# Optimization experiments

Hardware: AMD Instinct MI355X
Metric: run time of the kernel (lower is better)

The kernel has to match this reference:

```python
import jax, jax.numpy as jnp
import numpy as np
import math

N_HEADS = 16

def _rope_tables(T, D, dtype):
    # inv_freq over even dims, emb = [freqs, freqs] -> [T, D]
    inv_freq = 1.0 / (10000.0 ** (jnp.arange(0, D, 2, dtype=jnp.float32) / D))
    freqs = jnp.arange(T, dtype=jnp.float32)[:, None] * inv_freq[None, :]  # [T, D/2]
    emb = jnp.concatenate([freqs, freqs], axis=-1)  # [T, D]
    return jnp.cos(emb).astype(dtype), jnp.sin(emb).astype(dtype)

def _rotate_half(x):
    d = x.shape[-1] // 2
    return jnp.concatenate([-x[..., d:], x[..., :d]], axis=-1)

def setup_inputs() -> dict:
    key = jax.random.key(0)
    ks = jax.random.split(key, 5)
    B, T, C = 2, 2048, 1024
    s = 1.0 / math.sqrt(C)
    return {
        "x": jax.random.normal(ks[0], (B, T, C), dtype=jnp.float32),
        "Wq": jax.random.normal(ks[1], (C, C), dtype=jnp.float32) * s,
        "Wk": jax.random.normal(ks[2], (C, C), dtype=jnp.float32) * s,
        "Wv": jax.random.normal(ks[3], (C, C), dtype=jnp.float32) * s,
        "Wo": jax.random.normal(ks[4], (C, C), dtype=jnp.float32) * s,
    }

def reference(x, Wq, Wk, Wv, Wo):
    B, T, C = x.shape
    H = N_HEADS
    D = C // H
    # QKV projections (torch Linear, bias=False: y = x @ W.T), split into heads
    def proj(W):
        return (x @ W.T).reshape(B, T, H, D).transpose(0, 2, 1, 3)  # [B,H,T,D]
    q, k, v = proj(Wq), proj(Wk), proj(Wv)
    # RoPE
    cos, sin = _rope_tables(T, D, x.dtype)  # [T,D] each, broadcast over B,H
    q = q * cos + _rotate_half(q) * sin
    k = k * cos + _rotate_half(k) * sin
    # scaled dot-product attention with causal mask
    scale = 1.0 / math.sqrt(D)
    attn = jnp.einsum('bhtd,bhsd->bhts', q, k) * scale  # [B,H,T,T]
    row = jnp.arange(T)[:, None]
    col = jnp.arange(T)[None, :]
    attn = jnp.where(col > row, -jnp.inf, attn)
    p = jax.nn.softmax(attn, axis=-1)
    out = jnp.einsum('bhts,bhsd->bhtd', p, v)  # [B,H,T,D]
    out = out.transpose(0, 2, 1, 3).reshape(B, T, C)
    return out @ Wo.T
```

## Files before the change

### kernel.cpp

```cpp
#include <hip/hip_runtime.h>
#include <hip/hip_bf16.h>


typedef __hip_bfloat16 bf16;
typedef __attribute__((ext_vector_type(8))) short bf16x8;
typedef __attribute__((ext_vector_type(4))) float f32x4;
typedef __attribute__((ext_vector_type(4))) short short4v;

#define MFMA16(a, b, c) __builtin_amdgcn_mfma_f32_16x16x32_bf16((a), (b), (c), 0, 0, 0)

constexpr int Bn = 2, Hn = 16, Tn = 2048, Dn = 64, Cn = 1024;
constexpr size_t NE = (size_t)Bn * Tn * Cn;
constexpr size_t WE = (size_t)Cn * Cn;

__device__ inline unsigned short bfbits(float x) {
    bf16 b = __float2bfloat16(x);
    return *(unsigned short*)&b;
}

__device__ inline bf16x8 pack8(f32x4 a, f32x4 b) {
    bf16x8 r;
#pragma unroll
    for (int i = 0; i < 4; ++i) r[i] = (short)bfbits(a[i]);
#pragma unroll
    for (int i = 0; i < 4; ++i) r[4 + i] = (short)bfbits(b[i]);
    return r;
}

__device__ inline void gl_lds16(const bf16* g, unsigned short* l) {
    __builtin_amdgcn_global_load_lds(
        (const __attribute__((address_space(1))) void*)g,
        (__attribute__((address_space(3))) void*)l, 16, 0, 0);
}

__device__ inline void stage128(const bf16* gbase, int ld, unsigned short* lds,
                                int wave, int lane) {
#pragma unroll
    for (int j = 0; j < 4; ++j) {
        int p = j * 256 + wave * 64 + lane;
        int row = p >> 3, ch = (p & 7) ^ (row & 7);
        gl_lds16(gbase + (size_t)row * ld + ch * 8,
                 lds + (size_t)(j * 256 + wave * 64) * 8);
    }
}
__device__ inline void stage64(const bf16* gbase, int ld, unsigned short* lds,
                               int wave, int lane) {
#pragma unroll
    for (int j = 0; j < 2; ++j) {
        int p = j * 256 + wave * 64 + lane;
        int row = p >> 3, ch = (p & 7) ^ (row & 7);
        gl_lds16(gbase + (size_t)row * ld + ch * 8,
                 lds + (size_t)(j * 256 + wave * 64) * 8);
    }
}

__device__ inline bf16x8 ldsfrag(const unsigned short* base, int row, int ch) {
    return *(const bf16x8*)&base[row * 64 + ((ch ^ (row & 7)) * 8)];
}

__global__ __launch_bounds__(256) void convert_kernel(
    const float* __restrict__ x, const float* __restrict__ wq,
    const float* __restrict__ wk, const float* __restrict__ wv,
    const float* __restrict__ wo, bf16* __restrict__ dst)
{
    int blk = blockIdx.x;
    const float* src;
    size_t doff;
    if (blk < 2048) {
        src = x + (size_t)blk * 2048;
        doff = (size_t)blk * 2048;
    } else {
        int w = (blk - 2048) >> 9, b = (blk - 2048) & 511;
        const float* s4[4] = {wq, wk, wv, wo};
        src = s4[w] + (size_t)b * 2048;
        doff = NE + (size_t)w * WE + (size_t)b * 2048;
    }
    int t = threadIdx.x * 8;
    f32x4 a = *(const f32x4*)(src + t);
    f32x4 b2 = *(const f32x4*)(src + t + 4);
    *(bf16x8*)(dst + doff + t) = pack8(a, b2);
}

__global__ __launch_bounds__(256) void gemm_qkv_kernel(
    const bf16* __restrict__ X, const bf16* __restrict__ Wbase,
    bf16* __restrict__ Qo, bf16* __restrict__ Ko, bf16* __restrict__ Vo)
{
    __shared__ unsigned short As[128 * 64];
    __shared__ unsigned short Bs[128 * 64];
    const int bm = blockIdx.x, bn = blockIdx.y, wsel = blockIdx.z;
    const bf16* W = Wbase + (size_t)wsel * WE;
    const int tid  = threadIdx.x;
    const int wave = tid >> 6, lane = tid & 63;
    const int lx   = lane & 15, quad = lane >> 4;
    const int wm = wave >> 1, wn = wave & 1;

    const bf16* abase = X + (size_t)(bm * 128) * Cn;
    const bf16* bbase = W + (size_t)(bn * 128) * Cn;

    f32x4 acc[4][4] = {};
    for (int kt = 0; kt < Cn / 64; ++kt) {
        __syncthreads();
        stage128(abase + kt * 64, Cn, As, wave, lane);
        stage128(bbase + kt * 64, Cn, Bs, wave, lane);
        __syncthreads();
#pragma unroll
        for (int ks = 0; ks < 2; ++ks) {
            bf16x8 af[4], bfv[4];
#pragma unroll
            for (int mt = 0; mt < 4; ++mt)
                af[mt] = ldsfrag(As, wm * 64 + mt * 16 + lx, ks * 4 + quad);
#pragma unroll
            for (int nt = 0; nt < 4; ++nt)
                bfv[nt] = ldsfrag(Bs, wn * 64 + nt * 16 + lx, ks * 4 + quad);
#pragma unroll
            for (int mt = 0; mt < 4; ++mt)
#pragma unroll
                for (int nt = 0; nt < 4; ++nt)
                    acc[mt][nt] = MFMA16(af[mt], bfv[nt], acc[mt][nt]);
        }
    }

    const int h = bn * 2 + wn;
    if (wsel <= 1) {
#pragma unroll
        for (int mt = 0; mt < 4; ++mt)
#pragma unroll
            for (int r = 0; r < 4; ++r) {
                int mg = bm * 128 + wm * 64 + mt * 16 + quad * 4 + r;
                int t  = mg & (Tn - 1);
#pragma unroll
                for (int nt = 0; nt < 2; ++nt) {
                    int d = nt * 16 + lx;
                    float ang = (float)t * __expf(-(float)d * 0.2878231366f);
                    float c, s;
                    __sincosf(ang, &s, &c);
                    float a0 = acc[mt][nt][r], a1 = acc[mt][nt + 2][r];
                    acc[mt][nt][r]     = a0 * c - a1 * s;
                    acc[mt][nt + 2][r] = a1 * c + a0 * s;
                }
            }
    }

#pragma unroll
    for (int mt = 0; mt < 4; ++mt) {
        int mg0 = bm * 128 + wm * 64 + mt * 16 + quad * 4;
        int b = mg0 >> 11, t0 = mg0 & (Tn - 1);
        if (wsel == 0) {
#pragma unroll
            for (int nt = 0; nt < 4; ++nt)
#pragma unroll
                for (int r = 0; r < 4; ++r) {
                    int d = nt * 16 + lx;
                    Qo[((size_t)(b * Hn + h) * Tn + t0 + r) * Dn + d] =
                        __float2bfloat16(acc[mt][nt][r] * 0.125f);
                }
        } else if (wsel == 1) {
#pragma unroll
            for (int nt = 0; nt < 4; ++nt)
#pragma unroll
                for (int r = 0; r < 4; ++r) {
                    int d = nt * 16 + lx;
                    Ko[((size_t)(b * Hn + h) * Tn + t0 + r) * Dn + d] =
                        __float2bfloat16(acc[mt][nt][r]);
                }
        } else {
#pragma unroll
            for (int nt = 0; nt < 4; ++nt) {
                int d = nt * 16 + lx;
                short4v pk;
#pragma unroll
                for (int r = 0; r < 4; ++r) pk[r] = (short)bfbits(acc[mt][nt][r]);
                *(short4v*)&Vo[((size_t)(b * Hn + h) * Dn + d) * Tn + t0] = pk;
            }
        }
    }
}

__global__ __launch_bounds__(256) void gemm_out_kernel(
    const bf16* __restrict__ A, const bf16* __restrict__ W, float* __restrict__ Out)
{
    __shared__ unsigned short As[128 * 64];
    __shared__ unsigned short Bs[128 * 64];
    const int bm = blockIdx.x, bn = blockIdx.y;
    const int tid  = threadIdx.x;
    const int wave = tid >> 6, lane = tid & 63;
    const int lx   = lane & 15, quad = lane >> 4;
    const int wm = wave >> 1, wn = wave & 1;

    const bf16* abase = A + (size_t)(bm * 128) * Cn;
    const bf16* bbase = W + (size_t)(bn * 128) * Cn;

    f32x4 acc[4][4] = {};
    for (int kt = 0; kt < Cn / 64; ++kt) {
        __syncthreads();
        stage128(abase + kt * 64, Cn, As, wave, lane);
        stage128(bbase + kt * 64, Cn, Bs, wave, lane);
        __syncthreads();
#pragma unroll
        for (int ks = 0; ks < 2; ++ks) {
            bf16x8 af[4], bfv[4];
#pragma unroll
            for (int mt = 0; mt < 4; ++mt)
                af[mt] = ldsfrag(As, wm * 64 + mt * 16 + lx, ks * 4 + quad);
#pragma unroll
            for (int nt = 0; nt < 4; ++nt)
                bfv[nt] = ldsfrag(Bs, wn * 64 + nt * 16 + lx, ks * 4 + quad);
#pragma unroll
            for (int mt = 0; mt < 4; ++mt)
#pragma unroll
                for (int nt = 0; nt < 4; ++nt)
                    acc[mt][nt] = MFMA16(af[mt], bfv[nt], acc[mt][nt]);
        }
    }
#pragma unroll
    for (int mt = 0; mt < 4; ++mt)
#pragma unroll
        for (int nt = 0; nt < 4; ++nt)
#pragma unroll
            for (int r = 0; r < 4; ++r) {
                int mg = bm * 128 + wm * 64 + mt * 16 + quad * 4 + r;
                int ng = bn * 128 + wn * 64 + nt * 16 + lx;
                Out[(size_t)mg * Cn + ng] = acc[mt][nt][r];
            }
}

__device__ inline void attn_chunk(
    const unsigned short* Ks, const unsigned short* Vs, unsigned short* pw,
    bf16x8 aq0, bf16x8 aq1, bf16x8 ones, f32x4* acc_o, f32x4& acc_l,
    int row_local, bool masked, int lx, int quad)
{
    f32x4 accs[4] = {};
#pragma unroll
    for (int nt = 0; nt < 4; ++nt) {
        int key = nt * 16 + lx;
        bf16x8 k0 = ldsfrag(Ks, key, quad);
        bf16x8 k1 = ldsfrag(Ks, key, quad + 4);
        accs[nt] = MFMA16(aq0, k0, accs[nt]);
        accs[nt] = MFMA16(aq1, k1, accs[nt]);
    }
    if (!masked) {
#pragma unroll
        for (int nt = 0; nt < 4; ++nt)
#pragma unroll
            for (int r = 0; r < 4; ++r)
                pw[(quad * 4 + r) * 72 + nt * 16 + lx] = bfbits(__expf(accs[nt][r]));
    } else {
#pragma unroll
        for (int nt = 0; nt < 4; ++nt) {
            int keyl = nt * 16 + lx;
#pragma unroll
            for (int r = 0; r < 4; ++r) {
                float p = (keyl > row_local + r) ? 0.0f : __expf(accs[nt][r]);
                pw[(quad * 4 + r) * 72 + nt * 16 + lx] = bfbits(p);
            }
        }
    }
    asm volatile("s_waitcnt lgkmcnt(0)" ::: "memory");
    bf16x8 ap0 = *(const bf16x8*)&pw[lx * 72 + quad * 8];
    bf16x8 ap1 = *(const bf16x8*)&pw[lx * 72 + 32 + quad * 8];
    acc_l = MFMA16(ap0, ones, acc_l);
    acc_l = MFMA16(ap1, ones, acc_l);
#pragma unroll
    for (int dt = 0; dt < 4; ++dt) {
        int d = dt * 16 + lx;
        bf16x8 v0 = ldsfrag(Vs, d, quad);
        bf16x8 v1 = ldsfrag(Vs, d, quad + 4);
        acc_o[dt] = MFMA16(ap0, v0, acc_o[dt]);
        acc_o[dt] = MFMA16(ap1, v1, acc_o[dt]);
    }
}

__global__ __launch_bounds__(256) void attn_kernel(
    const bf16* __restrict__ Q, const bf16* __restrict__ K,
    const bf16* __restrict__ Vt, bf16* __restrict__ O)
{
    __shared__ unsigned short Ks[64 * 64];
    __shared__ unsigned short Vs[64 * 64];
    __shared__ unsigned short Pl[2][4][16 * 72];
    const int f = blockIdx.x;
    const int bh   = (f & 7) * 4 + (f >> 7);
    const int pair = (f >> 3) & 15;
    const int qlo = pair, qhi = 31 - pair;
    const int tid  = threadIdx.x;
    const int wave = tid >> 6, lane = tid & 63;
    const int lx   = lane & 15, quad = lane >> 4;

    const bf16* Qh = Q  + (size_t)bh * Tn * Dn;
    const bf16* Kh = K  + (size_t)bh * Tn * Dn;
    const bf16* Vh = Vt + (size_t)bh * Dn * Tn;

    const int rlo = qlo * 64 + wave * 16 + lx;
    const int rhi = qhi * 64 + wave * 16 + lx;
    bf16x8 aqlo0 = *(const bf16x8*)(Qh + (size_t)rlo * Dn + quad * 8);
    bf16x8 aqlo1 = *(const bf16x8*)(Qh + (size_t)rlo * Dn + 32 + quad * 8);
    bf16x8 aqhi0 = *(const bf16x8*)(Qh + (size_t)rhi * Dn + quad * 8);
    bf16x8 aqhi1 = *(const bf16x8*)(Qh + (size_t)rhi * Dn + 32 + quad * 8);

    bf16x8 ones;
#pragma unroll
    for (int i = 0; i < 8; ++i) ones[i] = (short)0x3F80;

    f32x4 acc_o[2][4] = {};
    f32x4 acc_l[2] = {};
    const int row_local = wave * 16 + quad * 4;

    for (int c = 0; c <= qhi; ++c) {
        __syncthreads();
        stage64(Kh + (size_t)c * 64 * Dn, Dn, Ks, wave, lane);
        stage64(Vh + (size_t)c * 64, Tn, Vs, wave, lane);
        __syncthreads();
        attn_chunk(Ks, Vs, &Pl[0][wave][0], aqhi0, aqhi1, ones,
                   acc_o[0], acc_l[0], row_local, c == qhi, lx, quad);
        if (c <= qlo)
            attn_chunk(Ks, Vs, &Pl[1][wave][0], aqlo0, aqlo1, ones,
                       acc_o[1], acc_l[1], row_local, c == qlo, lx, quad);
    }

    const int b = bh >> 4, h = bh & 15;
#pragma unroll
    for (int tile = 0; tile < 2; ++tile) {
        int qb = tile ? qlo : qhi;
#pragma unroll
        for (int dt = 0; dt < 4; ++dt)
#pragma unroll
            for (int r = 0; r < 4; ++r) {
                int t = qb * 64 + row_local + r;
                int d = dt * 16 + lx;
                float o = acc_o[tile][dt][r] / acc_l[tile][r];
                O[((size_t)(b * Tn + t) * Hn + h) * Dn + d] = __float2bfloat16(o);
            }
    }
}

extern "C" void kernel_launch(void* const* d_in, const int* in_sizes, int n_in,
                              void* d_out, int out_size, void* d_ws, size_t ws_size,
                              hipStream_t stream)
{
    const float* x  = (const float*)d_in[0];
    const float* Wq = (const float*)d_in[1];
    const float* Wk = (const float*)d_in[2];
    const float* Wv = (const float*)d_in[3];
    const float* Wo = (const float*)d_in[4];
    float* out = (float*)d_out;

    bf16* ws = (bf16*)d_ws;
    bf16* Xb = ws;
    bf16* Wb = ws + NE;
    bf16* Qb = ws + NE + 4 * WE;
    bf16* Kb = Qb + NE;
    bf16* Vb = Kb + NE;
    bf16* Ab = Xb;

    convert_kernel<<<4096, 256, 0, stream>>>(x, Wq, Wk, Wv, Wo, ws);
    gemm_qkv_kernel<<<dim3(32, 8, 3), 256, 0, stream>>>(Xb, Wb, Qb, Kb, Vb);
    attn_kernel<<<512, 256, 0, stream>>>(Qb, Kb, Vb, Ab);
    gemm_out_kernel<<<dim3(32, 8), 256, 0, stream>>>(Ab, Wb + 3 * WE, out);
}
```

Measured before the change: 187.6 us.

## Double-buffer LDS staging in GEMMs and attention, interleave hi/lo tile work

Both GEMM kernels switch from a 64-wide K tile with two barriers per step to a double-buffered 32-wide K tile with a rotated swizzle. The next tile is prefetched while MFMAs run on the current one, leaving one barrier per iteration. The attention kernel also double-buffers its K/V chunks and inlines the two query-tile passes so their score and PV MFMAs interleave and share K/V fragment loads. This trades more LDS use and more loop iterations for better overlap of global-to-LDS loads with compute.

```diff
diff --git a/kernel.cpp b/kernel.cpp
--- a/kernel.cpp
+++ b/kernel.cpp
@@ -33,16 +33,21 @@
         (__attribute__((address_space(3))) void*)l, 16, 0, 0);
 }
 
-__device__ inline void stage128(const bf16* gbase, int ld, unsigned short* lds,
-                                int wave, int lane) {
-#pragma unroll
-    for (int j = 0; j < 4; ++j) {
+__device__ inline void stage32(const bf16* gbase, int ld, unsigned short* lds,
+                               int wave, int lane) {
+#pragma unroll
+    for (int j = 0; j < 2; ++j) {
         int p = j * 256 + wave * 64 + lane;
-        int row = p >> 3, ch = (p & 7) ^ (row & 7);
+        int row = p >> 2;
+        int ch = ((p & 3) - (row >> 1)) & 3;
         gl_lds16(gbase + (size_t)row * ld + ch * 8,
                  lds + (size_t)(j * 256 + wave * 64) * 8);
     }
 }
+__device__ inline bf16x8 frag32(const unsigned short* base, int row, int q) {
+    return *(const bf16x8*)&base[row * 32 + (((q + (row >> 1)) & 3) * 8)];
+}
+
 __device__ inline void stage64(const bf16* gbase, int ld, unsigned short* lds,
                                int wave, int lane) {
 #pragma unroll
@@ -53,8 +58,7 @@
                  lds + (size_t)(j * 256 + wave * 64) * 8);
     }
 }
-
-__device__ inline bf16x8 ldsfrag(const unsigned short* base, int row, int ch) {
+__device__ inline bf16x8 frag64(const unsigned short* base, int row, int ch) {
     return *(const bf16x8*)&base[row * 64 + ((ch ^ (row & 7)) * 8)];
 }
 
@@ -85,8 +89,8 @@
     const bf16* __restrict__ X, const bf16* __restrict__ Wbase,
     bf16* __restrict__ Qo, bf16* __restrict__ Ko, bf16* __restrict__ Vo)
 {
-    __shared__ unsigned short As[128 * 64];
-    __shared__ unsigned short Bs[128 * 64];
+    __shared__ unsigned short As[2][128 * 32];
+    __shared__ unsigned short Bs[2][128 * 32];
     const int bm = blockIdx.x, bn = blockIdx.y, wsel = blockIdx.z;
     const bf16* W = Wbase + (size_t)wsel * WE;
     const int tid  = threadIdx.x;
@@ -98,26 +102,28 @@
     const bf16* bbase = W + (size_t)(bn * 128) * Cn;
 
     f32x4 acc[4][4] = {};
-    for (int kt = 0; kt < Cn / 64; ++kt) {
+    stage32(abase, Cn, As[0], wave, lane);
+    stage32(bbase, Cn, Bs[0], wave, lane);
+    for (int kt = 0; kt < 32; ++kt) {
         __syncthreads();
-        stage128(abase + kt * 64, Cn, As, wave, lane);
-        stage128(bbase + kt * 64, Cn, Bs, wave, lane);
-        __syncthreads();
-#pragma unroll
-        for (int ks = 0; ks < 2; ++ks) {
-            bf16x8 af[4], bfv[4];
-#pragma unroll
-            for (int mt = 0; mt < 4; ++mt)
-                af[mt] = ldsfrag(As, wm * 64 + mt * 16 + lx, ks * 4 + quad);
-#pragma unroll
-            for (int nt = 0; nt < 4; ++nt)
-                bfv[nt] = ldsfrag(Bs, wn * 64 + nt * 16 + lx, ks * 4 + quad);
-#pragma unroll
-            for (int mt = 0; mt < 4; ++mt)
-#pragma unroll
-                for (int nt = 0; nt < 4; ++nt)
-                    acc[mt][nt] = MFMA16(af[mt], bfv[nt], acc[mt][nt]);
-        }
+        if (kt < 31) {
+            stage32(abase + (kt + 1) * 32, Cn, As[(kt + 1) & 1], wave, lane);
+            stage32(bbase + (kt + 1) * 32, Cn, Bs[(kt + 1) & 1], wave, lane);
+        }
+        const unsigned short* as = As[kt & 1];
+        const unsigned short* bs = Bs[kt & 1];
+        bf16x8 af[4], bfv[4];
+#pragma unroll
+        for (int mt = 0; mt < 4; ++mt)
+            af[mt] = frag32(as, wm * 64 + mt * 16 + lx, quad);
+#pragma unroll
+        for (int nt = 0; nt < 4; ++nt)
+            bfv[nt] = frag32(bs, wn * 64 + nt * 16 + lx, quad);
+#pragma unroll
+        for (int mt = 0; mt < 4; ++mt)
+#pragma unroll
+            for (int nt = 0; nt < 4; ++nt)
+                acc[mt][nt] = MFMA16(af[mt], bfv[nt], acc[mt][nt]);
     }
 
     const int h = bn * 2 + wn;
@@ -179,8 +185,8 @@
 __global__ __launch_bounds__(256) void gemm_out_kernel(
     const bf16* __restrict__ A, const bf16* __restrict__ W, float* __restrict__ Out)
 {
-    __shared__ unsigned short As[128 * 64];
-    __shared__ unsigned short Bs[128 * 64];
+    __shared__ unsigned short As[2][128 * 32];
+    __shared__ unsigned short Bs[2][128 * 32];
     const int bm = blockIdx.x, bn = blockIdx.y;
     const int tid  = threadIdx.x;
     const int wave = tid >> 6, lane = tid & 63;
@@ -191,26 +197,28 @@
     const bf16* bbase = W + (size_t)(bn * 128) * Cn;
 
     f32x4 acc[4][4] = {};
-    for (int kt = 0; kt < Cn / 64; ++kt) {
+    stage32(abase, Cn, As[0], wave, lane);
+    stage32(bbase, Cn, Bs[0], wave, lane);
+    for (int kt = 0; kt < 32; ++kt) {
         __syncthreads();
-        stage128(abase + kt * 64, Cn, As, wave, lane);
-        stage128(bbase + kt * 64, Cn, Bs, wave, lane);
-        __syncthreads();
-#pragma unroll
-        for (int ks = 0; ks < 2; ++ks) {
-            bf16x8 af[4], bfv[4];
-#pragma unroll
-            for (int mt = 0; mt < 4; ++mt)
-                af[mt] = ldsfrag(As, wm * 64 + mt * 16 + lx, ks * 4 + quad);
-#pragma unroll
-            for (int nt = 0; nt < 4; ++nt)
-                bfv[nt] = ldsfrag(Bs, wn * 64 + nt * 16 + lx, ks * 4 + quad);
-#pragma unroll
-            for (int mt = 0; mt < 4; ++mt)
-#pragma unroll
-                for (int nt = 0; nt < 4; ++nt)
-                    acc[mt][nt] = MFMA16(af[mt], bfv[nt], acc[mt][nt]);
-        }
+        if (kt < 31) {
+            stage32(abase + (kt + 1) * 32, Cn, As[(kt + 1) & 1], wave, lane);
+            stage32(bbase + (kt + 1) * 32, Cn, Bs[(kt + 1) & 1], wave, lane);
+        }
+        const unsigned short* as = As[kt & 1];
+        const unsigned short* bs = Bs[kt & 1];
+        bf16x8 af[4], bfv[4];
+#pragma unroll
+        for (int mt = 0; mt < 4; ++mt)
+            af[mt] = frag32(as, wm * 64 + mt * 16 + lx, quad);
+#pragma unroll
+        for (int nt = 0; nt < 4; ++nt)
+            bfv[nt] = frag32(bs, wn * 64 + nt * 16 + lx, quad);
+#pragma unroll
+        for (int mt = 0; mt < 4; ++mt)
+#pragma unroll
+            for (int nt = 0; nt < 4; ++nt)
+                acc[mt][nt] = MFMA16(af[mt], bfv[nt], acc[mt][nt]);
     }
 #pragma unroll
     for (int mt = 0; mt < 4; ++mt)
@@ -224,58 +232,12 @@
             }
 }
 
-__device__ inline void attn_chunk(
-    const unsigned short* Ks, const unsigned short* Vs, unsigned short* pw,
-    bf16x8 aq0, bf16x8 aq1, bf16x8 ones, f32x4* acc_o, f32x4& acc_l,
-    int row_local, bool masked, int lx, int quad)
-{
-    f32x4 accs[4] = {};
-#pragma unroll
-    for (int nt = 0; nt < 4; ++nt) {
-        int key = nt * 16 + lx;
-        bf16x8 k0 = ldsfrag(Ks, key, quad);
-        bf16x8 k1 = ldsfrag(Ks, key, quad + 4);
-        accs[nt] = MFMA16(aq0, k0, accs[nt]);
-        accs[nt] = MFMA16(aq1, k1, accs[nt]);
-    }
-    if (!masked) {
-#pragma unroll
-        for (int nt = 0; nt < 4; ++nt)
-#pragma unroll
-            for (int r = 0; r < 4; ++r)
-                pw[(quad * 4 + r) * 72 + nt * 16 + lx] = bfbits(__expf(accs[nt][r]));
-    } else {
-#pragma unroll
-        for (int nt = 0; nt < 4; ++nt) {
-            int keyl = nt * 16 + lx;
-#pragma unroll
-            for (int r = 0; r < 4; ++r) {
-                float p = (keyl > row_local + r) ? 0.0f : __expf(accs[nt][r]);
-                pw[(quad * 4 + r) * 72 + nt * 16 + lx] = bfbits(p);
-            }
-        }
-    }
-    asm volatile("s_waitcnt lgkmcnt(0)" ::: "memory");
-    bf16x8 ap0 = *(const bf16x8*)&pw[lx * 72 + quad * 8];
-    bf16x8 ap1 = *(const bf16x8*)&pw[lx * 72 + 32 + quad * 8];
-    acc_l = MFMA16(ap0, ones, acc_l);
-    acc_l = MFMA16(ap1, ones, acc_l);
-#pragma unroll
-    for (int dt = 0; dt < 4; ++dt) {
-        int d = dt * 16 + lx;
-        bf16x8 v0 = ldsfrag(Vs, d, quad);
-        bf16x8 v1 = ldsfrag(Vs, d, quad + 4);
-        acc_o[dt] = MFMA16(ap0, v0, acc_o[dt]);
-        acc_o[dt] = MFMA16(ap1, v1, acc_o[dt]);
-    }
-}
-
 __global__ __launch_bounds__(256) void attn_kernel(
     const bf16* __restrict__ Q, const bf16* __restrict__ K,
     const bf16* __restrict__ Vt, bf16* __restrict__ O)
 {
-    __shared__ unsigned short Ks[64 * 64];
-    __shared__ unsigned short Vs[64 * 64];
+    __shared__ unsigned short Ks[2][64 * 64];
+    __shared__ unsigned short Vs[2][64 * 64];
     __shared__ unsigned short Pl[2][4][16 * 72];
     const int f = blockIdx.x;
     const int bh   = (f & 7) * 4 + (f >> 7);
@@ -303,17 +265,94 @@
     f32x4 acc_o[2][4] = {};
     f32x4 acc_l[2] = {};
     const int row_local = wave * 16 + quad * 4;
-
+    unsigned short* phi = &Pl[0][wave][0];
+    unsigned short* plo = &Pl[1][wave][0];
+
+    stage64(Kh, Dn, Ks[0], wave, lane);
+    stage64(Vh, Tn, Vs[0], wave, lane);
     for (int c = 0; c <= qhi; ++c) {
         __syncthreads();
-        stage64(Kh + (size_t)c * 64 * Dn, Dn, Ks, wave, lane);
-        stage64(Vh + (size_t)c * 64, Tn, Vs, wave, lane);
-        __syncthreads();
-        attn_chunk(Ks, Vs, &Pl[0][wave][0], aqhi0, aqhi1, ones,
-                   acc_o[0], acc_l[0], row_local, c == qhi, lx, quad);
-        if (c <= qlo)
-            attn_chunk(Ks, Vs, &Pl[1][wave][0], aqlo0, aqlo1, ones,
-                       acc_o[1], acc_l[1], row_local, c == qlo, lx, quad);
+        if (c < qhi) {
+            stage64(Kh + (size_t)(c + 1) * 64 * Dn, Dn, Ks[(c + 1) & 1], wave, lane);
+            stage64(Vh + (size_t)(c + 1) * 64, Tn, Vs[(c + 1) & 1], wave, lane);
+        }
+        const unsigned short* ks = Ks[c & 1];
+        const unsigned short* vs = Vs[c & 1];
+        const bool do_lo = (c <= qlo);
+
+        f32x4 shi[4] = {}, slo[4] = {};
+#pragma unroll
+        for (int nt = 0; nt < 4; ++nt) {
+            int key = nt * 16 + lx;
+            bf16x8 k0 = frag64(ks, key, quad);
+            bf16x8 k1 = frag64(ks, key, quad + 4);
+            shi[nt] = MFMA16(aqhi0, k0, shi[nt]);
+            shi[nt] = MFMA16(aqhi1, k1, shi[nt]);
+            if (do_lo) {
+                slo[nt] = MFMA16(aqlo0, k0, slo[nt]);
+                slo[nt] = MFMA16(aqlo1, k1, slo[nt]);
+            }
+        }
+        if (c < qhi) {
+#pragma unroll
+            for (int nt = 0; nt < 4; ++nt)
+#pragma unroll
+                for (int r = 0; r < 4; ++r)
+                    phi[(quad * 4 + r) * 72 + nt * 16 + lx] = bfbits(__expf(shi[nt][r]));
+        } else {
+#pragma unroll
+            for (int nt = 0; nt < 4; ++nt) {
+                int keyl = nt * 16 + lx;
+#pragma unroll
+                for (int r = 0; r < 4; ++r) {
+                    float p = (keyl > row_local + r) ? 0.0f : __expf(shi[nt][r]);
+                    phi[(quad * 4 + r) * 72 + nt * 16 + lx] = bfbits(p);
+                }
+            }
+        }
+        if (do_lo) {
+            if (c < qlo) {
+#pragma unroll
+                for (int nt = 0; nt < 4; ++nt)
+#pragma unroll
+                    for (int r = 0; r < 4; ++r)
+                        plo[(quad * 4 + r) * 72 + nt * 16 + lx] = bfbits(__expf(slo[nt][r]));
+            } else {
+#pragma unroll
+                for (int nt = 0; nt < 4; ++nt) {
+                    int keyl = nt * 16 + lx;
+#pragma unroll
+                    for (int r = 0; r < 4; ++r) {
+                        float p = (keyl > row_local + r) ? 0.0f : __expf(slo[nt][r]);
+                        plo[(quad * 4 + r) * 72 + nt * 16 + lx] = bfbits(p);
+                    }
+                }
+            }
+        }
+        asm volatile("s_waitcnt lgkmcnt(0)" ::: "memory");
+        bf16x8 aph0 = *(const bf16x8*)&phi[lx * 72 + quad * 8];
+        bf16x8 aph1 = *(const bf16x8*)&phi[lx * 72 + 32 + quad * 8];
+        acc_l[0] = MFMA16(aph0, ones, acc_l[0]);
+        acc_l[0] = MFMA16(aph1, ones, acc_l[0]);
+        bf16x8 apl0, apl1;
+        if (do_lo) {
+            apl0 = *(const bf16x8*)&plo[lx * 72 + quad * 8];
+            apl1 = *(const bf16x8*)&plo[lx * 72 + 32 + quad * 8];
+            acc_l[1] = MFMA16(apl0, ones, acc_l[1]);
+            acc_l[1] = MFMA16(apl1, ones, acc_l[1]);
+        }
+#pragma unroll
+        for (int dt = 0; dt < 4; ++dt) {
+            int d = dt * 16 + lx;
+            bf16x8 v0 = frag64(vs, d, quad);
+            bf16x8 v1 = frag64(vs, d, quad + 4);
+            acc_o[0][dt] = MFMA16(aph0, v0, acc_o[0][dt]);
+            acc_o[0][dt] = MFMA16(aph1, v1, acc_o[0][dt]);
+            if (do_lo) {
+                acc_o[1][dt] = MFMA16(apl0, v0, acc_o[1][dt]);
+                acc_o[1][dt] = MFMA16(apl1, v1, acc_o[1][dt]);
+            }
+        }
     }
 
     const int b = bh >> 4, h = bh & 15;
```

Result: slower. 212.1 us (+13.0%).

## Split attention into one query tile per block and narrow output GEMM tiles

Applied to the files above, without the earlier changes.

The attention kernel stops pairing a low and a high query tile in each block. It now launches 1024 blocks, each handling one 64-row query tile, and orders them longest-first so the load stays balanced. The output projection GEMM goes from 128x128 to 128x64 tiles, which doubles the grid to 512 blocks. Both changes raise the block count to fill the MI355X's compute units, at the cost of reloading K/V tiles more often across blocks and doubling how many times the A tile is staged in the out GEMM.

```diff
diff --git a/kernel.cpp b/kernel.cpp
--- a/kernel.cpp
+++ b/kernel.cpp
@@ -180,7 +180,7 @@
     const bf16* __restrict__ A, const bf16* __restrict__ W, float* __restrict__ Out)
 {
     __shared__ unsigned short As[128 * 64];
-    __shared__ unsigned short Bs[128 * 64];
+    __shared__ unsigned short Bs[64 * 64];
     const int bm = blockIdx.x, bn = blockIdx.y;
     const int tid  = threadIdx.x;
     const int wave = tid >> 6, lane = tid & 63;
@@ -188,86 +188,40 @@
     const int wm = wave >> 1, wn = wave & 1;
 
     const bf16* abase = A + (size_t)(bm * 128) * Cn;
-    const bf16* bbase = W + (size_t)(bn * 128) * Cn;
-
-    f32x4 acc[4][4] = {};
+    const bf16* bbase = W + (size_t)(bn * 64) * Cn;
+
+    f32x4 acc[4][2] = {};
     for (int kt = 0; kt < Cn / 64; ++kt) {
         __syncthreads();
         stage128(abase + kt * 64, Cn, As, wave, lane);
-        stage128(bbase + kt * 64, Cn, Bs, wave, lane);
+        stage64(bbase + kt * 64, Cn, Bs, wave, lane);
         __syncthreads();
 #pragma unroll
         for (int ks = 0; ks < 2; ++ks) {
-            bf16x8 af[4], bfv[4];
+            bf16x8 af[4], bfv[2];
 #pragma unroll
             for (int mt = 0; mt < 4; ++mt)
                 af[mt] = ldsfrag(As, wm * 64 + mt * 16 + lx, ks * 4 + quad);
 #pragma unroll
-            for (int nt = 0; nt < 4; ++nt)
-                bfv[nt] = ldsfrag(Bs, wn * 64 + nt * 16 + lx, ks * 4 + quad);
+            for (int nt = 0; nt < 2; ++nt)
+                bfv[nt] = ldsfrag(Bs, wn * 32 + nt * 16 + lx, ks * 4 + quad);
 #pragma unroll
             for (int mt = 0; mt < 4; ++mt)
 #pragma unroll
-                for (int nt = 0; nt < 4; ++nt)
+                for (int nt = 0; nt < 2; ++nt)
                     acc[mt][nt] = MFMA16(af[mt], bfv[nt], acc[mt][nt]);
         }
     }
 #pragma unroll
     for (int mt = 0; mt < 4; ++mt)
 #pragma unroll
-        for (int nt = 0; nt < 4; ++nt)
+        for (int nt = 0; nt < 2; ++nt)
 #pragma unroll
             for (int r = 0; r < 4; ++r) {
                 int mg = bm * 128 + wm * 64 + mt * 16 + quad * 4 + r;
-                int ng = bn * 128 + wn * 64 + nt * 16 + lx;
+                int ng = bn * 64 + wn * 32 + nt * 16 + lx;
                 Out[(size_t)mg * Cn + ng] = acc[mt][nt][r];
             }
-}
-
-__device__ inline void attn_chunk(
-    const unsigned short* Ks, const unsigned short* Vs, unsigned short* pw,
-    bf16x8 aq0, bf16x8 aq1, bf16x8 ones, f32x4* acc_o, f32x4& acc_l,
-    int row_local, bool masked, int lx, int quad)
-{
-    f32x4 accs[4] = {};
-#pragma unroll
-    for (int nt = 0; nt < 4; ++nt) {
-        int key = nt * 16 + lx;
-        bf16x8 k0 = ldsfrag(Ks, key, quad);
-        bf16x8 k1 = ldsfrag(Ks, key, quad + 4);
-        accs[nt] = MFMA16(aq0, k0, accs[nt]);
-        accs[nt] = MFMA16(aq1, k1, accs[nt]);
-    }
-    if (!masked) {
-#pragma unroll
-        for (int nt = 0; nt < 4; ++nt)
-#pragma unroll
-            for (int r = 0; r < 4; ++r)
-                pw[(quad * 4 + r) * 72 + nt * 16 + lx] = bfbits(__expf(accs[nt][r]));
-    } else {
-#pragma unroll
-        for (int nt = 0; nt < 4; ++nt) {
-            int keyl = nt * 16 + lx;
-#pragma unroll
-            for (int r = 0; r < 4; ++r) {
-                float p = (keyl > row_local + r) ? 0.0f : __expf(accs[nt][r]);
-                pw[(quad * 4 + r) * 72 + nt * 16 + lx] = bfbits(p);
-            }
-        }
-    }
-    asm volatile("s_waitcnt lgkmcnt(0)" ::: "memory");
-    bf16x8 ap0 = *(const bf16x8*)&pw[lx * 72 + quad * 8];
-    bf16x8 ap1 = *(const bf16x8*)&pw[lx * 72 + 32 + quad * 8];
-    acc_l = MFMA16(ap0, ones, acc_l);
-    acc_l = MFMA16(ap1, ones, acc_l);
-#pragma unroll
-    for (int dt = 0; dt < 4; ++dt) {
-        int d = dt * 16 + lx;
-        bf16x8 v0 = ldsfrag(Vs, d, quad);
-        bf16x8 v1 = ldsfrag(Vs, d, quad + 4);
-        acc_o[dt] = MFMA16(ap0, v0, acc_o[dt]);
-        acc_o[dt] = MFMA16(ap1, v1, acc_o[dt]);
-    }
 }
 
 __global__ __launch_bounds__(256) void attn_kernel(
@@ -276,11 +230,10 @@
 {
     __shared__ unsigned short Ks[64 * 64];
     __shared__ unsigned short Vs[64 * 64];
-    __shared__ unsigned short Pl[2][4][16 * 72];
-    const int f = blockIdx.x;
-    const int bh   = (f & 7) * 4 + (f >> 7);
-    const int pair = (f >> 3) & 15;
-    const int qlo = pair, qhi = 31 - pair;
+    __shared__ unsigned short Pl[4][16 * 72];
+    const int f  = blockIdx.x;
+    const int bh = (f & 7) * 4 + ((f >> 3) & 3);
+    const int qb = 31 - (f >> 5);
     const int tid  = threadIdx.x;
     const int wave = tid >> 6, lane = tid & 63;
     const int lx   = lane & 15, quad = lane >> 4;
@@ -288,48 +241,76 @@
     const bf16* Qh = Q  + (size_t)bh * Tn * Dn;
     const bf16* Kh = K  + (size_t)bh * Tn * Dn;
     const bf16* Vh = Vt + (size_t)bh * Dn * Tn;
-
-    const int rlo = qlo * 64 + wave * 16 + lx;
-    const int rhi = qhi * 64 + wave * 16 + lx;
-    bf16x8 aqlo0 = *(const bf16x8*)(Qh + (size_t)rlo * Dn + quad * 8);
-    bf16x8 aqlo1 = *(const bf16x8*)(Qh + (size_t)rlo * Dn + 32 + quad * 8);
-    bf16x8 aqhi0 = *(const bf16x8*)(Qh + (size_t)rhi * Dn + quad * 8);
-    bf16x8 aqhi1 = *(const bf16x8*)(Qh + (size_t)rhi * Dn + 32 + quad * 8);
+    unsigned short* pw = &Pl[wave][0];
+
+    const int qrowA = qb * 64 + wave * 16 + lx;
+    bf16x8 aq0 = *(const bf16x8*)(Qh + (size_t)qrowA * Dn + quad * 8);
+    bf16x8 aq1 = *(const bf16x8*)(Qh + (size_t)qrowA * Dn + 32 + quad * 8);
 
     bf16x8 ones;
 #pragma unroll
     for (int i = 0; i < 8; ++i) ones[i] = (short)0x3F80;
 
-    f32x4 acc_o[2][4] = {};
-    f32x4 acc_l[2] = {};
+    f32x4 acc_o[4] = {};
+    f32x4 acc_l = {};
     const int row_local = wave * 16 + quad * 4;
 
-    for (int c = 0; c <= qhi; ++c) {
+    for (int c = 0; c <= qb; ++c) {
         __syncthreads();
         stage64(Kh + (size_t)c * 64 * Dn, Dn, Ks, wave, lane);
         stage64(Vh + (size_t)c * 64, Tn, Vs, wave, lane);
         __syncthreads();
-        attn_chunk(Ks, Vs, &Pl[0][wave][0], aqhi0, aqhi1, ones,
-                   acc_o[0], acc_l[0], row_local, c == qhi, lx, quad);
-        if (c <= qlo)
-            attn_chunk(Ks, Vs, &Pl[1][wave][0], aqlo0, aqlo1, ones,
-                       acc_o[1], acc_l[1], row_local, c == qlo, lx, quad);
+        f32x4 accs[4] = {};
+#pragma unroll
+        for (int nt = 0; nt < 4; ++nt) {
+            int key = nt * 16 + lx;
+            bf16x8 k0 = ldsfrag(Ks, key, quad);
+            bf16x8 k1 = ldsfrag(Ks, key, quad + 4);
+            accs[nt] = MFMA16(aq0, k0, accs[nt]);
+            accs[nt] = MFMA16(aq1, k1, accs[nt]);
+        }
+        if (c < qb) {
+#pragma unroll
+            for (int nt = 0; nt < 4; ++nt)
+#pragma unroll
+                for (int r = 0; r < 4; ++r)
+                    pw[(quad * 4 + r) * 72 + nt * 16 + lx] = bfbits(__expf(accs[nt][r]));
+        } else {
+#pragma unroll
+            for (int nt = 0; nt < 4; ++nt) {
+                int keyl = nt * 16 + lx;
+#pragma unroll
+                for (int r = 0; r < 4; ++r) {
+                    float p = (keyl > row_local + r) ? 0.0f : __expf(accs[nt][r]);
+                    pw[(quad * 4 + r) * 72 + nt * 16 + lx] = bfbits(p);
+                }
+            }
+        }
+        asm volatile("s_waitcnt lgkmcnt(0)" ::: "memory");
+        bf16x8 ap0 = *(const bf16x8*)&pw[lx * 72 + quad * 8];
+        bf16x8 ap1 = *(const bf16x8*)&pw[lx * 72 + 32 + quad * 8];
+        acc_l = MFMA16(ap0, ones, acc_l);
+        acc_l = MFMA16(ap1, ones, acc_l);
+#pragma unroll
+        for (int dt = 0; dt < 4; ++dt) {
+            int d = dt * 16 + lx;
+            bf16x8 v0 = ldsfrag(Vs, d, quad);
+            bf16x8 v1 = ldsfrag(Vs, d, quad + 4);
+            acc_o[dt] = MFMA16(ap0, v0, acc_o[dt]);
+            acc_o[dt] = MFMA16(ap1, v1, acc_o[dt]);
+        }
     }
 
     const int b = bh >> 4, h = bh & 15;
 #pragma unroll
-    for (int tile = 0; tile < 2; ++tile) {
-        int qb = tile ? qlo : qhi;
-#pragma unroll
-        for (int dt = 0; dt < 4; ++dt)
-#pragma unroll
-            for (int r = 0; r < 4; ++r) {
-                int t = qb * 64 + row_local + r;
-                int d = dt * 16 + lx;
-                float o = acc_o[tile][dt][r] / acc_l[tile][r];
-                O[((size_t)(b * Tn + t) * Hn + h) * Dn + d] = __float2bfloat16(o);
-            }
-    }
+    for (int dt = 0; dt < 4; ++dt)
+#pragma unroll
+        for (int r = 0; r < 4; ++r) {
+            int t = qb * 64 + row_local + r;
+            int d = dt * 16 + lx;
+            float o = acc_o[dt][r] / acc_l[r];
+            O[((size_t)(b * Tn + t) * Hn + h) * Dn + d] = __float2bfloat16(o);
+        }
 }
 
 extern "C" void kernel_launch(void* const* d_in, const int* in_sizes, int n_in,
@@ -353,6 +334,6 @@
 
     convert_kernel<<<4096, 256, 0, stream>>>(x, Wq, Wk, Wv, Wo, ws);
     gemm_qkv_kernel<<<dim3(32, 8, 3), 256, 0, stream>>>(Xb, Wb, Qb, Kb, Vb);
-    attn_kernel<<<512, 256, 0, stream>>>(Qb, Kb, Vb, Ab);
-    gemm_out_kernel<<<dim3(32, 8), 256, 0, stream>>>(Ab, Wb + 3 * WE, out);
-}
+    attn_kernel<<<1024, 256, 0, stream>>>(Qb, Kb, Vb, Ab);
+    gemm_out_kernel<<<dim3(32, 16), 256, 0, stream>>>(Ab, Wb + 3 * WE, out);
+}
```

New measurement: 177.4 us. 5.4% less time.
